# Performance work log

Hardware: AMD Instinct MI355X
Metric: run time of the kernel (lower is better)

The kernel has to match this reference:

```python
import jax, jax.numpy as jnp
import numpy as np

N_NODES = 10000
W_DIM = 512
N_EDGES = 200000


def setup_inputs() -> dict:
    key = jax.random.key(0)
    k1, k2, k3 = jax.random.split(key, 3)
    z_drug = jax.random.normal(k1, (N_NODES, W_DIM), dtype=jnp.float32)
    # glorot-style init for the bilinear weight
    glorot_std = jnp.sqrt(2.0 / (W_DIM + W_DIM)).astype(jnp.float32)
    weight = jax.random.normal(k2, (W_DIM, W_DIM), dtype=jnp.float32) * glorot_std
    batch_edges = jax.random.randint(k3, (2, N_EDGES), 0, N_NODES, dtype=jnp.int64)
    return {"z_drug": z_drug, "weight": weight, "batch_edges": batch_edges}


def reference(z_drug, weight, batch_edges):
    # edge_type == 'drug_drug': both endpoints come from the drug table.
    row_embed = z_drug[batch_edges[0]]  # [E, d]
    col_embed = z_drug[batch_edges[1]]  # [E, d]
    # score_e = row_e @ W @ col_e  == diag((Z1 W) Z2^T) without the N x N blowup
    score = jnp.einsum('ed,df,ef->e', row_embed, weight, col_embed)
    return jax.nn.sigmoid(score)  # is_sigmoid=True default
```

## Files before the change

### kernel.cpp

```cpp
#include <hip/hip_runtime.h>
#include <math.h>

#define DIM     512
#define NNODES  10000
#define NEDGES  200000
#define MPAD    10048
#define NMB     157

using short8  = __attribute__((ext_vector_type(8))) short;
using floatx4 = __attribute__((ext_vector_type(4))) float;
using half8   = __attribute__((ext_vector_type(8))) _Float16;
using half2v  = __attribute__((ext_vector_type(2))) _Float16;

__device__ inline float dot2acc(half2v a, half2v b, float c) {
#if __has_builtin(__builtin_amdgcn_fdot2)
    return __builtin_amdgcn_fdot2(a, b, c, false);
#else
    return fmaf((float)a[0], (float)b[0], fmaf((float)a[1], (float)b[1], c));
#endif
}

#define PREP_ZBLK 2512
__global__ __launch_bounds__(256) void prep(const float* __restrict__ Z,
                                            const float* __restrict__ W,
                                            _Float16* __restrict__ Zh16,
                                            _Float16* __restrict__ Wh16t,
                                            int* __restrict__ counts) {
    const int b = blockIdx.x;
    const int t = threadIdx.x;

    if (b < 40) {
        int i = b * 256 + t;
        if (i < NNODES) counts[i] = 0;
    }

    if (b < PREP_ZBLK) {
        const int idx8 = (b * 256 + t) * 8;
        const int m = idx8 >> 9;
        float x[8];
        if (m < NNODES) {
            float4 v0 = *(const float4*)(Z + idx8);
            float4 v1 = *(const float4*)(Z + idx8 + 4);
            x[0]=v0.x; x[1]=v0.y; x[2]=v0.z; x[3]=v0.w;
            x[4]=v1.x; x[5]=v1.y; x[6]=v1.z; x[7]=v1.w;
        } else {
            #pragma unroll
            for (int j = 0; j < 8; ++j) x[j] = 0.f;
        }
        half8 h;
        #pragma unroll
        for (int j = 0; j < 8; ++j) h[j] = (_Float16)x[j];
        *(half8*)(Zh16 + idx8) = h;
    } else {
        __shared__ float tile[64][65];
        const int wb = b - PREP_ZBLK;
        const int kb = (wb >> 3) * 64;
        const int nb = (wb & 7) * 64;
        const int kk = t >> 2;
        const int ch = t & 3;

        const float* src = W + (size_t)(kb + kk) * DIM + nb + ch * 16;
        #pragma unroll
        for (int q = 0; q < 4; ++q) {
            float4 v = *(const float4*)(src + q * 4);
            tile[kk][ch * 16 + q * 4 + 0] = v.x;
            tile[kk][ch * 16 + q * 4 + 1] = v.y;
            tile[kk][ch * 16 + q * 4 + 2] = v.z;
            tile[kk][ch * 16 + q * 4 + 3] = v.w;
        }
        __syncthreads();

        const int nn = kk;
        half8 h0, h1;
        #pragma unroll
        for (int i = 0; i < 8; ++i) h0[i] = (_Float16)tile[ch * 16 + i][nn];
        #pragma unroll
        for (int i = 0; i < 8; ++i) h1[i] = (_Float16)tile[ch * 16 + 8 + i][nn];
        _Float16* d = Wh16t + (size_t)(nb + nn) * DIM + kb + ch * 16;
        *(half8*)(d)     = h0;
        *(half8*)(d + 8) = h1;
    }
}

__global__ __launch_bounds__(256) void gemm_f16(const _Float16* __restrict__ Zh16,
                                                const _Float16* __restrict__ Wh16t,
                                                _Float16* __restrict__ ZWh) {
    __shared__ _Float16 Abuf[2][64 * 32];
    __shared__ _Float16 Bbuf[2][128 * 32];

    const int t     = threadIdx.x;
    const int bid   = blockIdx.x;
    const int n_idx = bid & 3;
    const int m0    = (bid >> 2) * 64;
    const int n0    = n_idx * 128;

    const int l  = t & 63;
    const int w  = t >> 6;
    const int wn = w * 32;
    const int lm = l & 15;
    const int lq = l >> 4;
    const unsigned wbase = (unsigned)(t & 192);

    floatx4 acc[4][2] = {};

    const int arow = t >> 2;
    const int ach  = t & 3;

    auto stage = [&](int buf, int k0) {
        {
            const _Float16* s = Zh16 + (size_t)(m0 + arow) * DIM + k0 + ach * 8;
            __builtin_amdgcn_global_load_lds(
                (const __attribute__((address_space(1))) void*)s,
                (__attribute__((address_space(3))) void*)&Abuf[buf][wbase * 8], 16, 0, 0);
        }
        #pragma unroll
        for (int p = 0; p < 2; ++p) {
            const int sidx = p * 256 + t;
            const int row  = sidx >> 2;
            const int ch   = sidx & 3;
            const _Float16* s = Wh16t + (size_t)(n0 + row) * DIM + k0 + ch * 8;
            __builtin_amdgcn_global_load_lds(
                (const __attribute__((address_space(1))) void*)s,
                (__attribute__((address_space(3))) void*)&Bbuf[buf][(p * 256 + wbase) * 8], 16, 0, 0);
        }
    };

    stage(0, 0);
    __syncthreads();

    for (int s = 0; s < 16; ++s) {
        const int buf = s & 1;
        if (s < 15) stage(buf ^ 1, (s + 1) * 32);

        half8 aF[4], bF[2];
        #pragma unroll
        for (int i = 0; i < 4; ++i)
            aF[i] = *(const half8*)&Abuf[buf][(16 * i + lm) * 32 + lq * 8];
        #pragma unroll
        for (int j = 0; j < 2; ++j)
            bF[j] = *(const half8*)&Bbuf[buf][(wn + 16 * j + lm) * 32 + lq * 8];

        #pragma unroll
        for (int i = 0; i < 4; ++i)
            #pragma unroll
            for (int j = 0; j < 2; ++j)
                acc[i][j] = __builtin_amdgcn_mfma_f32_16x16x32_f16(aF[i], bF[j], acc[i][j], 0, 0, 0);

        __syncthreads();
    }

    #pragma unroll
    for (int i = 0; i < 4; ++i)
        #pragma unroll
        for (int j = 0; j < 2; ++j)
            #pragma unroll
            for (int r = 0; r < 4; ++r) {
                const int gm = m0 + 16 * i + lq * 4 + r;
                const int gn = n0 + wn + 16 * j + lm;
                if (gm < NNODES)
                    ZWh[(size_t)gm * DIM + gn] = (_Float16)acc[i][j][r];
            }
}

__global__ void hist_rows(const int* __restrict__ eidx, int* __restrict__ counts) {
    int e = blockIdx.x * blockDim.x + threadIdx.x;
    if (e < NEDGES) atomicAdd(&counts[eidx[e]], 1);
}

__global__ __launch_bounds__(1024) void scan_counts(const int* __restrict__ counts,
                                                    int* __restrict__ offs,
                                                    int* __restrict__ cursor) {
    __shared__ int wsum[16];
    __shared__ int woff[17];
    const int t    = threadIdx.x;
    const int lane = t & 63;
    const int wv   = t >> 6;

    int local[10];
    int s = 0;
    if (t < 1000) {
        #pragma unroll
        for (int j = 0; j < 10; ++j) {
            local[j] = counts[t * 10 + j];
            s += local[j];
        }
    }
    int v = s;
    #pragma unroll
    for (int off = 1; off < 64; off <<= 1) {
        int u = __shfl_up(v, off, 64);
        if (lane >= off) v += u;
    }
    if (lane == 63) wsum[wv] = v;
    __syncthreads();
    if (t == 0) {
        int r = 0;
        #pragma unroll
        for (int i = 0; i < 16; ++i) { woff[i] = r; r += wsum[i]; }
        woff[16] = r;
    }
    __syncthreads();
    if (t < 1000) {
        int run = woff[wv] + (v - s);
        #pragma unroll
        for (int j = 0; j < 10; ++j) {
            offs[t * 10 + j]   = run;
            cursor[t * 10 + j] = run;
            run += local[j];
        }
    }
    if (t == 0) offs[NNODES] = woff[16];
}

__global__ void scatter_edges(const int* __restrict__ eidx,
                              int* __restrict__ cursor,
                              unsigned* __restrict__ keys) {
    int e = blockIdx.x * blockDim.x + threadIdx.x;
    if (e < NEDGES) {
        int r = eidx[e];
        int c = eidx[NEDGES + e];
        int pos = atomicAdd(&cursor[r], 1);
        keys[pos] = ((unsigned)c << 18) | (unsigned)e;
    }
}

__global__ __launch_bounds__(256) void edge_score_q(const _Float16* __restrict__ ZWh,
                                                    const _Float16* __restrict__ Zh,
                                                    const unsigned* __restrict__ keys,
                                                    const int* __restrict__ offs,
                                                    float* __restrict__ out) {
    const int r = blockIdx.x * 4 + (threadIdx.x >> 6);
    const int start = offs[r];
    const int end   = offs[r + 1];
    if (start == end) return;

    const int lane = threadIdx.x & 63;
    const int g    = lane >> 4;
    const int sl   = lane & 15;

    const _Float16* rp = ZWh + (size_t)r * DIM + sl * 32;
    half8 ra0 = *(const half8*)(rp);
    half8 ra1 = *(const half8*)(rp + 8);
    half8 ra2 = *(const half8*)(rp + 16);
    half8 ra3 = *(const half8*)(rp + 24);

    for (int i = start; i < end; i += 4) {
        const int ii = i + g;
        const unsigned k = keys[ii < end ? ii : (end - 1)];
        const int c = (int)(k >> 18);

        const _Float16* cp = Zh + (size_t)c * DIM + sl * 32;
        half8 c0 = *(const half8*)(cp);
        half8 c1 = *(const half8*)(cp + 8);
        half8 c2 = *(const half8*)(cp + 16);
        half8 c3 = *(const half8*)(cp + 24);

        float s = 0.f;
        #pragma unroll
        for (int d = 0; d < 4; ++d) {
            s = dot2acc((half2v){ra0[2*d], ra0[2*d+1]}, (half2v){c0[2*d], c0[2*d+1]}, s);
            s = dot2acc((half2v){ra1[2*d], ra1[2*d+1]}, (half2v){c1[2*d], c1[2*d+1]}, s);
            s = dot2acc((half2v){ra2[2*d], ra2[2*d+1]}, (half2v){c2[2*d], c2[2*d+1]}, s);
            s = dot2acc((half2v){ra3[2*d], ra3[2*d+1]}, (half2v){c3[2*d], c3[2*d+1]}, s);
        }

        s += __shfl_xor(s, 1, 64);
        s += __shfl_xor(s, 2, 64);
        s += __shfl_xor(s, 4, 64);
        s += __shfl_xor(s, 8, 64);

        if (sl == 0 && ii < end)
            out[k & 0x3FFFFu] = 1.0f / (1.0f + expf(-s));
    }
}

#define GTM 128
#define GTN 64
#define GTK 16
#define LDA 132
#define LDB 68

__global__ __launch_bounds__(256) void gemm_zw(const float* __restrict__ A,
                                               const float* __restrict__ B,
                                               float* __restrict__ C) {
    __shared__ float As[GTK * LDA];
    __shared__ float Bs[GTK * LDB];

    const int t  = threadIdx.x;
    const int m0 = blockIdx.x * GTM;
    const int n0 = blockIdx.y * GTN;
    const int tx = t & 15;
    const int ty = t >> 4;

    float acc[8][4] = {};

    for (int k0 = 0; k0 < DIM; k0 += GTK) {
        #pragma unroll
        for (int p = 0; p < 2; ++p) {
            int f  = t + p * 256;
            int mm = f >> 2;
            int kq = f & 3;
            int m  = m0 + mm;
            float4 v = make_float4(0.f, 0.f, 0.f, 0.f);
            if (m < NNODES)
                v = *(const float4*)(A + (size_t)m * DIM + k0 + kq * 4);
            As[(kq * 4 + 0) * LDA + mm] = v.x;
            As[(kq * 4 + 1) * LDA + mm] = v.y;
            As[(kq * 4 + 2) * LDA + mm] = v.z;
            As[(kq * 4 + 3) * LDA + mm] = v.w;
        }
        {
            int kb = t >> 4, n4 = t & 15;
            *(float4*)&Bs[kb * LDB + n4 * 4] =
                *(const float4*)(B + (size_t)(k0 + kb) * DIM + n0 + n4 * 4);
        }
        __syncthreads();

        #pragma unroll
        for (int kk = 0; kk < GTK; ++kk) {
            float4 a0 = *(const float4*)&As[kk * LDA + ty * 8];
            float4 a1 = *(const float4*)&As[kk * LDA + ty * 8 + 4];
            float4 b  = *(const float4*)&Bs[kk * LDB + tx * 4];
            float av[8] = {a0.x, a0.y, a0.z, a0.w, a1.x, a1.y, a1.z, a1.w};
            float bv[4] = {b.x, b.y, b.z, b.w};
            #pragma unroll
            for (int i = 0; i < 8; ++i)
                #pragma unroll
                for (int j = 0; j < 4; ++j)
                    acc[i][j] = fmaf(av[i], bv[j], acc[i][j]);
        }
        __syncthreads();
    }

    #pragma unroll
    for (int i = 0; i < 8; ++i) {
        int m = m0 + ty * 8 + i;
        if (m < NNODES)
            *(float4*)(C + (size_t)m * DIM + n0 + tx * 4) =
                make_float4(acc[i][0], acc[i][1], acc[i][2], acc[i][3]);
    }
}

__global__ __launch_bounds__(256) void edge_score(const float* __restrict__ ZW,
                                                  const float* __restrict__ Z,
                                                  const int* __restrict__ eidx,
                                                  float* __restrict__ out) {
    const int e    = blockIdx.x * 4 + (threadIdx.x >> 6);
    const int lane = threadIdx.x & 63;

    const int r = eidx[e];
    const int c = eidx[NEDGES + e];

    const float4* pr = (const float4*)(ZW + (size_t)r * DIM);
    const float4* pc = (const float4*)(Z  + (size_t)c * DIM);

    float4 a0 = pr[lane * 2 + 0];
    float4 a1 = pr[lane * 2 + 1];
    float4 b0 = pc[lane * 2 + 0];
    float4 b1 = pc[lane * 2 + 1];

    float s = a0.x * b0.x;
    s = fmaf(a0.y, b0.y, s);
    s = fmaf(a0.z, b0.z, s);
    s = fmaf(a0.w, b0.w, s);
    s = fmaf(a1.x, b1.x, s);
    s = fmaf(a1.y, b1.y, s);
    s = fmaf(a1.z, b1.z, s);
    s = fmaf(a1.w, b1.w, s);

    #pragma unroll
    for (int off = 32; off > 0; off >>= 1)
        s += __shfl_xor(s, off, 64);

    if (lane == 0)
        out[e] = 1.0f / (1.0f + expf(-s));
}

extern "C" void kernel_launch(void* const* d_in, const int* in_sizes, int n_in,
                              void* d_out, int out_size, void* d_ws, size_t ws_size,
                              hipStream_t stream) {
    const float* Z  = (const float*)d_in[0];
    const float* W  = (const float*)d_in[1];
    const int*   EI = (const int*)d_in[2];
    float* out = (float*)d_out;

    char* p = (char*)d_ws;
    _Float16* ZWh   = (_Float16*)p;  p += (size_t)MPAD * DIM * 2;
    _Float16* Zh16  = (_Float16*)p;  p += (size_t)MPAD * DIM * 2;
    _Float16* Wh16t = (_Float16*)p;  p += (size_t)DIM * DIM * 2;
    int* counts = (int*)p;           p += (size_t)NNODES * 4;
    int* offs   = (int*)p;           p += (size_t)(NNODES + 1) * 4;
    int* cursor = (int*)p;           p += (size_t)NNODES * 4;
    unsigned* keys = (unsigned*)p;   p += (size_t)NEDGES * 4;
    const size_t need_full = (size_t)(p - (char*)d_ws);

    if (ws_size >= need_full) {
        prep<<<PREP_ZBLK + 64, 256, 0, stream>>>(Z, W, Zh16, Wh16t, counts);
        gemm_f16<<<NMB * 4, 256, 0, stream>>>(Zh16, Wh16t, ZWh);
        hist_rows<<<(NEDGES + 255) / 256, 256, 0, stream>>>(EI, counts);
        scan_counts<<<1, 1024, 0, stream>>>(counts, offs, cursor);
        scatter_edges<<<(NEDGES + 255) / 256, 256, 0, stream>>>(EI, cursor, keys);
        edge_score_q<<<NNODES / 4, 256, 0, stream>>>(ZWh, Zh16, keys, offs, out);
    } else {
        float* ZW = (float*)d_ws;
        dim3 g1((NNODES + GTM - 1) / GTM, DIM / GTN);
        gemm_zw<<<g1, 256, 0, stream>>>(Z, W, ZW);
        edge_score<<<NEDGES / 4, 256, 0, stream>>>(ZW, Z, EI, out);
    }
}
```

Baseline: 145.8 us.

## Bucket edges by column-index group so each pass gathers a smaller column range

Edges are now bucketed by (column index >> 11, row) instead of by row alone, giving five column groups of up to 2048 nodes each. The scoring kernel launches one wave per (group, row) bucket. Blocks that run at the same time therefore gather columns from a roughly 2 MB slice of the fp16 table, which should raise L2 hit rates for the random column reads. The cost is that each row's ZW vector is loaded up to five times, the count/offset arrays and the scan grow fivefold, and the single-block scan now runs a serial loop of 49 elements per thread.

```diff
diff --git a/kernel.cpp b/kernel.cpp
--- a/kernel.cpp
+++ b/kernel.cpp
@@ -6,6 +6,8 @@
 #define NEDGES  200000
 #define MPAD    10048
 #define NMB     157
+#define NGRP    5
+#define NB      (NGRP * NNODES)
 
 using short8  = __attribute__((ext_vector_type(8))) short;
 using floatx4 = __attribute__((ext_vector_type(4))) float;
@@ -29,9 +31,9 @@
     const int b = blockIdx.x;
     const int t = threadIdx.x;
 
-    if (b < 40) {
+    if (b < 196) {
         int i = b * 256 + t;
-        if (i < NNODES) counts[i] = 0;
+        if (i < NB) counts[i] = 0;
     }
 
     if (b < PREP_ZBLK) {
@@ -164,7 +166,11 @@
 
 __global__ void hist_rows(const int* __restrict__ eidx, int* __restrict__ counts) {
     int e = blockIdx.x * blockDim.x + threadIdx.x;
-    if (e < NEDGES) atomicAdd(&counts[eidx[e]], 1);
+    if (e < NEDGES) {
+        int r = eidx[e];
+        int c = eidx[NEDGES + e];
+        atomicAdd(&counts[(c >> 11) * NNODES + r], 1);
+    }
 }
 
 __global__ __launch_bounds__(1024) void scan_counts(const int* __restrict__ counts,
@@ -176,15 +182,12 @@
     const int lane = t & 63;
     const int wv   = t >> 6;
 
-    int local[10];
+    const int lo = t * 49;
+    const int hi = min(lo + 49, NB);
+
     int s = 0;
-    if (t < 1000) {
-        #pragma unroll
-        for (int j = 0; j < 10; ++j) {
-            local[j] = counts[t * 10 + j];
-            s += local[j];
-        }
-    }
+    for (int i = lo; i < hi; ++i) s += counts[i];
+
     int v = s;
     #pragma unroll
     for (int off = 1; off < 64; off <<= 1) {
@@ -200,16 +203,14 @@
         woff[16] = r;
     }
     __syncthreads();
-    if (t < 1000) {
-        int run = woff[wv] + (v - s);
-        #pragma unroll
-        for (int j = 0; j < 10; ++j) {
-            offs[t * 10 + j]   = run;
-            cursor[t * 10 + j] = run;
-            run += local[j];
-        }
-    }
-    if (t == 0) offs[NNODES] = woff[16];
+
+    int run = woff[wv] + (v - s);
+    for (int i = lo; i < hi; ++i) {
+        offs[i]   = run;
+        cursor[i] = run;
+        run += counts[i];
+    }
+    if (t == 0) offs[NB] = woff[16];
 }
 
 __global__ void scatter_edges(const int* __restrict__ eidx,
@@ -219,7 +220,7 @@
     if (e < NEDGES) {
         int r = eidx[e];
         int c = eidx[NEDGES + e];
-        int pos = atomicAdd(&cursor[r], 1);
+        int pos = atomicAdd(&cursor[(c >> 11) * NNODES + r], 1);
         keys[pos] = ((unsigned)c << 18) | (unsigned)e;
     }
 }
@@ -229,13 +230,16 @@
                                                     const unsigned* __restrict__ keys,
                                                     const int* __restrict__ offs,
                                                     float* __restrict__ out) {
-    const int r = blockIdx.x * 4 + (threadIdx.x >> 6);
-    const int start = offs[r];
-    const int end   = offs[r + 1];
+    const int b = blockIdx.x * 4 + (threadIdx.x >> 6);
+    const int start = offs[b];
+    const int end   = offs[b + 1];
     if (start == end) return;
 
+    const unsigned g = (unsigned)b / NNODES;
+    const int r = b - (int)g * NNODES;
+
     const int lane = threadIdx.x & 63;
-    const int g    = lane >> 4;
+    const int gq   = lane >> 4;
     const int sl   = lane & 15;
 
     const _Float16* rp = ZWh + (size_t)r * DIM + sl * 32;
@@ -245,7 +249,7 @@
     half8 ra3 = *(const half8*)(rp + 24);
 
     for (int i = start; i < end; i += 4) {
-        const int ii = i + g;
+        const int ii = i + gq;
         const unsigned k = keys[ii < end ? ii : (end - 1)];
         const int c = (int)(k >> 18);
 
@@ -388,9 +392,9 @@
     _Float16* ZWh   = (_Float16*)p;  p += (size_t)MPAD * DIM * 2;
     _Float16* Zh16  = (_Float16*)p;  p += (size_t)MPAD * DIM * 2;
     _Float16* Wh16t = (_Float16*)p;  p += (size_t)DIM * DIM * 2;
-    int* counts = (int*)p;           p += (size_t)NNODES * 4;
-    int* offs   = (int*)p;           p += (size_t)(NNODES + 1) * 4;
-    int* cursor = (int*)p;           p += (size_t)NNODES * 4;
+    int* counts = (int*)p;           p += (size_t)NB * 4;
+    int* offs   = (int*)p;           p += (size_t)(NB + 1) * 4;
+    int* cursor = (int*)p;           p += (size_t)NB * 4;
     unsigned* keys = (unsigned*)p;   p += (size_t)NEDGES * 4;
     const size_t need_full = (size_t)(p - (char*)d_ws);
 
@@ -400,7 +404,7 @@
         hist_rows<<<(NEDGES + 255) / 256, 256, 0, stream>>>(EI, counts);
         scan_counts<<<1, 1024, 0, stream>>>(counts, offs, cursor);
         scatter_edges<<<(NEDGES + 255) / 256, 256, 0, stream>>>(EI, cursor, keys);
-        edge_score_q<<<NNODES / 4, 256, 0, stream>>>(ZWh, Zh16, keys, offs, out);
+        edge_score_q<<<NB / 4, 256, 0, stream>>>(ZWh, Zh16, keys, offs, out);
     } else {
         float* ZW = (float*)d_ws;
         dim3 g1((NNODES + GTM - 1) / GTM, DIM / GTN);
```

New measurement: 245.6 us. +68.5%, slower.
